# Optimization experiments

Hardware: AMD Instinct MI355X
Metric: run time of the kernel (lower is better)

Reference implementation:

```python
import jax, jax.numpy as jnp
import numpy as np

B, S = 8, 2048
E1, E2, E3 = 256, 256, 512
E = E1 + E2 + E3
NEG_SLOPE = 0.2


def setup_inputs() -> dict:
    key = jax.random.key(0)
    ks = jax.random.split(key, 11)
    scale = 1.0 / np.sqrt(E)
    return {
        "embeding1": jax.random.normal(ks[0], (B, S, E1), jnp.float32),
        "embeding2": jax.random.normal(ks[1], (B, S, E2), jnp.float32),
        "embeding3": jax.random.normal(ks[2], (B, S, E3), jnp.float32),
        # nn.Linear weights are [out, in]; apply as x @ W.T + b
        "Wq": jax.random.uniform(ks[3], (E, E), jnp.float32, -scale, scale),
        "bq": jax.random.uniform(ks[4], (E,), jnp.float32, -scale, scale),
        "Wk": jax.random.uniform(ks[5], (E, E), jnp.float32, -scale, scale),
        "bk": jax.random.uniform(ks[6], (E,), jnp.float32, -scale, scale),
        "Wv": jax.random.uniform(ks[7], (E, E), jnp.float32, -scale, scale),
        "bv": jax.random.uniform(ks[8], (E,), jnp.float32, -scale, scale),
        "Wf": jax.random.uniform(ks[9], (E, E), jnp.float32, -scale, scale),
        "bf": jax.random.uniform(ks[10], (E,), jnp.float32, -scale, scale),
    }


def reference(embeding1, embeding2, embeding3, Wq, bq, Wk, bk, Wv, bv, Wf, bf):
    x = jnp.concatenate([embeding1, embeding2, embeding3], axis=-1)  # [B,S,E]
    q = jnp.einsum("bse,oe->bso", x, Wq) + bq
    k = jnp.einsum("bse,oe->bso", x, Wk) + bk
    v = jnp.einsum("bse,oe->bso", x, Wv) + bv
    # NOTE: no 1/sqrt(d) scaling, faithful to the original module
    scores = jnp.einsum("bqe,bke->bqk", q, k)  # [B,S,S]
    probs = jax.nn.softmax(scores, axis=-1)
    weighted = jnp.einsum("bqk,bke->bqe", probs, v)  # [B,S,E]
    out = jnp.einsum("bse,oe->bso", weighted, Wf) + bf
    return jnp.where(out >= 0, out, NEG_SLOPE * out)
```

## Files before the change

### kernel.cpp

```cpp
#include <hip/hip_runtime.h>
#include <hip/hip_fp16.h>

typedef _Float16 half8 __attribute__((ext_vector_type(8)));
typedef _Float16 half4v __attribute__((ext_vector_type(4)));
typedef float floatx4 __attribute__((ext_vector_type(4)));

__device__ __forceinline__ void load_lds16(const void* g, void* l) {
    __builtin_amdgcn_global_load_lds(
        (const __attribute__((address_space(1))) void*)g,
        (__attribute__((address_space(3))) void*)l,
        16, 0, 0);
}

__device__ __forceinline__ void stage_half(const _Float16* g, long ld, _Float16* dst) {
    const int t = threadIdx.x;
#pragma unroll
    for (int j = 0; j < 2; ++j) {
        const int c = j * 512 + t;
        const int row = c >> 3;
        const int slot = (c & 7) ^ (row & 7);
        load_lds16(g + (long)row * ld + slot * 8, dst + c * 8);
    }
}

#define GEMM_PRELUDE                                                               \
    const int lane = threadIdx.x & 63;                                             \
    const int w    = threadIdx.x >> 6;                                             \
    const int wr   = w >> 2;                                                       \
    const int wc   = w & 3;                                                        \
    const int rsel = lane & 15, gsel = lane >> 4;                                  \
    const int NT = K >> 6;                                                         \
    (void)lane;
#define STAGE(BUF, KT)                                                             \
    stage_half(A + (KT) * 64, lda, lds + (BUF) * 32768);                           \
    stage_half(A + (long)128 * lda + (KT) * 64, lda, lds + (BUF) * 32768 + 8192);  \
    stage_half(B + (KT) * 64, ldb, lds + (BUF) * 32768 + 16384);                   \
    stage_half(B + (long)128 * ldb + (KT) * 64, ldb, lds + (BUF) * 32768 + 24576);
#define READ_A(dst, AH, MH)                                                        \
    _Pragma("unroll") for (int mi = 0; mi < 4; ++mi) {                             \
        const int r = ((MH) * 4 + mi) * 16 + rsel;                                 \
        dst[mi][0] = *(const half8*)&(AH)[r * 64 + ((gsel ^ (r & 7)) << 3)];       \
        dst[mi][1] = *(const half8*)&(AH)[r * 64 + (((4 + gsel) ^ (r & 7)) << 3)]; \
    }
#define READ_B(dst, BH, NH)                                                        \
    _Pragma("unroll") for (int ni = 0; ni < 2; ++ni) {                             \
        const int rn = (wc & 1) * 64 + ((NH) * 2 + ni) * 16 + rsel;                \
        dst[ni][0] = *(const half8*)&(BH)[rn * 64 + ((gsel ^ (rn & 7)) << 3)];     \
        dst[ni][1] = *(const half8*)&(BH)[rn * 64 + (((4 + gsel) ^ (rn & 7)) << 3)]; \
    }
#define MFMA_Q(MH, NH, A_, B_)                                                     \
    _Pragma("unroll") for (int mi = 0; mi < 4; ++mi)                               \
    _Pragma("unroll") for (int ni = 0; ni < 2; ++ni) {                             \
        acc[(MH) * 4 + mi][(NH) * 2 + ni] = __builtin_amdgcn_mfma_f32_16x16x32_f16( \
            A_[mi][0], B_[ni][0], acc[(MH) * 4 + mi][(NH) * 2 + ni], 0, 0, 0);     \
        acc[(MH) * 4 + mi][(NH) * 2 + ni] = __builtin_amdgcn_mfma_f32_16x16x32_f16( \
            A_[mi][1], B_[ni][1], acc[(MH) * 4 + mi][(NH) * 2 + ni], 0, 0, 0);     \
    }
#define SB0 __builtin_amdgcn_sched_barrier(0)

__device__ __forceinline__ void gemm256_core(const _Float16* A, long lda,
                                             const _Float16* B, long ldb,
                                             int K, floatx4 acc[8][4],
                                             _Float16* lds) {
    GEMM_PRELUDE
    half8 a_lo[4][2], a_hi[4][2], b_lo[2][2], b_hi[2][2];
    STAGE(0, 0);
    asm volatile("s_waitcnt vmcnt(0)" ::: "memory");
    __builtin_amdgcn_s_barrier();
    SB0;
#pragma unroll 1
    for (int t = 0; t < NT; ++t) {
        const int buf = t & 1;
        if (t + 1 < NT) { STAGE(buf ^ 1, t + 1); }
        const _Float16* Ah = lds + buf * 32768 + wr * 8192;
        const _Float16* Bh = lds + buf * 32768 + 16384 + (wc >> 1) * 8192;
        READ_A(a_lo, Ah, 0);
        READ_B(b_lo, Bh, 0);
        SB0;
        READ_A(a_hi, Ah, 1);
        SB0;
        READ_B(b_hi, Bh, 1);
        asm volatile("s_waitcnt lgkmcnt(12)" ::: "memory");
        SB0;
        MFMA_Q(0, 0, a_lo, b_lo);
        asm volatile("s_waitcnt lgkmcnt(4)" ::: "memory");
        SB0;
        MFMA_Q(1, 0, a_hi, b_lo);
        asm volatile("s_waitcnt lgkmcnt(0)" ::: "memory");
        SB0;
        MFMA_Q(0, 1, a_lo, b_hi);
        MFMA_Q(1, 1, a_hi, b_hi);
        asm volatile("s_waitcnt vmcnt(0)" ::: "memory");
        __builtin_amdgcn_s_barrier();
        SB0;
    }
}

__device__ __forceinline__ void gemm256_core_pv(const _Float16* A, long lda,
                                                const _Float16* B, long ldb,
                                                int K, floatx4 acc[8][4],
                                                _Float16* lds, const float* scl) {
    GEMM_PRELUDE
    half8 a_lo[4][2], a_hi[4][2], b_lo[2][2], b_hi[2][2];
    STAGE(0, 0);
    asm volatile("s_waitcnt vmcnt(0)" ::: "memory");
    __builtin_amdgcn_s_barrier();
    SB0;
#pragma unroll 1
    for (int t = 0; t < NT; ++t) {
        const int buf = t & 1;
        if (t + 1 < NT) { STAGE(buf ^ 1, t + 1); }
        const _Float16* Ah = lds + buf * 32768 + wr * 8192;
        const _Float16* Bh = lds + buf * 32768 + 16384 + (wc >> 1) * 8192;
        const float* srow = scl + (t >> 2) * 256 + wr * 128 + rsel;
        float s_lo[4], s_hi[4];
#pragma unroll
        for (int mi = 0; mi < 4; ++mi) s_lo[mi] = srow[mi * 16];
#pragma unroll
        for (int mi = 0; mi < 4; ++mi) s_hi[mi] = srow[64 + mi * 16];
        SB0;
        READ_A(a_lo, Ah, 0);
        READ_B(b_lo, Bh, 0);
        SB0;
        READ_A(a_hi, Ah, 1);
        SB0;
        READ_B(b_hi, Bh, 1);
        asm volatile("s_waitcnt lgkmcnt(12)" ::: "memory");
        SB0;
#pragma unroll
        for (int mi = 0; mi < 4; ++mi) {
            const _Float16 h = (_Float16)s_lo[mi];
            a_lo[mi][0] = a_lo[mi][0] * h;
            a_lo[mi][1] = a_lo[mi][1] * h;
        }
        MFMA_Q(0, 0, a_lo, b_lo);
        asm volatile("s_waitcnt lgkmcnt(4)" ::: "memory");
        SB0;
#pragma unroll
        for (int mi = 0; mi < 4; ++mi) {
            const _Float16 h = (_Float16)s_hi[mi];
            a_hi[mi][0] = a_hi[mi][0] * h;
            a_hi[mi][1] = a_hi[mi][1] * h;
        }
        MFMA_Q(1, 0, a_hi, b_lo);
        asm volatile("s_waitcnt lgkmcnt(0)" ::: "memory");
        SB0;
        MFMA_Q(0, 1, a_lo, b_hi);
        MFMA_Q(1, 1, a_hi, b_hi);
        asm volatile("s_waitcnt vmcnt(0)" ::: "memory");
        __builtin_amdgcn_s_barrier();
        SB0;
    }
}

__device__ __forceinline__ void zero_acc8(floatx4 acc[8][4]) {
    const floatx4 z = {0.f, 0.f, 0.f, 0.f};
#pragma unroll
    for (int m = 0; m < 8; ++m)
#pragma unroll
        for (int n = 0; n < 4; ++n) acc[m][n] = z;
}


__global__ __launch_bounds__(256) void prep_kernel(const float* e1, const float* e2,
                                                   const float* e3, const float* Wq,
                                                   const float* Wk, const float* Wv,
                                                   const float* Wf, _Float16* X,
                                                   _Float16* Wdst) {
    const int bid = blockIdx.x;
    if (bid < 16384) {
        long i = ((long)bid * 256 + threadIdx.x) * 4;
        int m = (int)(i >> 10);
        int c = (int)(i & 1023);
        const float* src;
        if (c < 256)      src = e1 + (long)m * 256 + c;
        else if (c < 512) src = e2 + (long)m * 256 + (c - 256);
        else              src = e3 + (long)m * 512 + (c - 512);
        float4 f = *(const float4*)src;
        half4v h;
        h[0] = (_Float16)f.x; h[1] = (_Float16)f.y;
        h[2] = (_Float16)f.z; h[3] = (_Float16)f.w;
        *(half4v*)&X[i] = h;
    } else {
        long i = ((long)(bid - 16384) * 256 + threadIdx.x) * 4;
        int which = (int)(i >> 20);
        long off = i & 1048575;
        const float* w = which == 0 ? Wq : which == 1 ? Wk : which == 2 ? Wv : Wf;
        float4 f = *(const float4*)(w + off);
        half4v h;
        h[0] = (_Float16)f.x; h[1] = (_Float16)f.y;
        h[2] = (_Float16)f.z; h[3] = (_Float16)f.w;
        *(half4v*)&Wdst[i] = h;
    }
}

__global__ __launch_bounds__(512, 2) void qkv_kernel(const _Float16* X, const _Float16* W,
                                                     const float* bq, const float* bk,
                                                     const float* bv, _Float16* q,
                                                     _Float16* k, _Float16* vT) {
    extern __shared__ _Float16 lds[];
    const int m0 = blockIdx.x * 256;
    const int n0 = blockIdx.y * 256;
    const int z  = blockIdx.z;
    floatx4 acc[8][4];
    zero_acc8(acc);
    gemm256_core(X + (long)m0 * 1024, 1024,
                 W + (long)z * 1048576 + (long)n0 * 1024, 1024, 1024, acc, lds);

    const float* bias = (z == 0) ? bq : (z == 1) ? bk : bv;
    const int lane = threadIdx.x & 63;
    const int w = threadIdx.x >> 6;
    const int wr = w >> 2, wc = w & 3;
    const int rsel = lane & 15, gsel = lane >> 4;

    if (z == 2) {
        const int rb = wr * 128 + gsel * 4;
        const int cb = wc * 64 + rsel;
#pragma unroll
        for (int mI = 0; mI < 8; ++mI) {
#pragma unroll
            for (int nI = 0; nI < 4; ++nI) {
                const int c = cb + nI * 16;
                const int r = rb + mI * 16;
                const float bb = bias[n0 + c];
                half4v vv;
#pragma unroll
                for (int j = 0; j < 4; ++j) vv[j] = (_Float16)(acc[mI][nI][j] + bb);
                *(half4v*)&lds[c * 256 + (r ^ ((c & 7) << 3))] = vv;
            }
        }
        __syncthreads();
#pragma unroll
        for (int it = 0; it < 16; ++it) {
            const int idx = it * 512 + threadIdx.x;
            const int c = idx >> 5;
            const int mc = idx & 31;
            half8 v = *(const half8*)&lds[c * 256 + ((mc * 8) ^ ((c & 7) << 3))];
            *(half8*)&vT[(long)(n0 + c) * 16384 + m0 + mc * 8] = v;
        }
    } else {
        _Float16* dst = (z == 0) ? q : k;
        const int r0 = m0 + wr * 128 + gsel * 4;
        const int c0 = n0 + wc * 64 + rsel;
#pragma unroll
        for (int mI = 0; mI < 8; ++mI) {
#pragma unroll
            for (int nI = 0; nI < 4; ++nI) {
                const int r = r0 + mI * 16;
                const int c = c0 + nI * 16;
                const float bb = bias[c];
#pragma unroll
                for (int j = 0; j < 4; ++j)
                    dst[(long)(r + j) * 1024 + c] = (_Float16)(acc[mI][nI][j] + bb);
            }
        }
    }
}

__global__ __launch_bounds__(512, 2) void scores_kernel(const _Float16* qh,
                                                        const _Float16* kh,
                                                        _Float16* es, float* tmax,
                                                        float* tsum) {
    extern __shared__ _Float16 lds[];
    const int m0 = blockIdx.x * 256;
    const int n0 = blockIdx.y * 256;
    const int tile = blockIdx.y;
    const int b = blockIdx.z;
    floatx4 acc[8][4];
    zero_acc8(acc);
    gemm256_core(qh + ((long)b * 2048 + m0) * 1024, 1024,
                 kh + ((long)b * 2048 + n0) * 1024, 1024, 1024, acc, lds);

    const int lane = threadIdx.x & 63;
    const int w = threadIdx.x >> 6;
    const int wr = w >> 2, wc = w & 3;
    const int rsel = lane & 15, gsel = lane >> 4;
    float* red = (float*)lds;

    float mx[8][4];
#pragma unroll
    for (int m = 0; m < 8; ++m)
#pragma unroll
        for (int j = 0; j < 4; ++j) {
            float v = acc[m][0][j];
#pragma unroll
            for (int n = 1; n < 4; ++n) v = fmaxf(v, acc[m][n][j]);
#pragma unroll
            for (int d = 1; d < 16; d <<= 1) v = fmaxf(v, __shfl_xor(v, d));
            mx[m][j] = v;
        }
    if (rsel == 0) {
#pragma unroll
        for (int m = 0; m < 8; ++m)
#pragma unroll
            for (int j = 0; j < 4; ++j)
                red[(wr * 128 + m * 16 + gsel * 4 + j) * 4 + wc] = mx[m][j];
    }
    __syncthreads();
#pragma unroll
    for (int m = 0; m < 8; ++m)
#pragma unroll
        for (int j = 0; j < 4; ++j) {
            const int row = wr * 128 + m * 16 + gsel * 4 + j;
            float4 rv = *(const float4*)&red[row * 4];
            mx[m][j] = fmaxf(fmaxf(rv.x, rv.y), fmaxf(rv.z, rv.w));
        }
    __syncthreads();

    float sm[8][4];
#pragma unroll
    for (int m = 0; m < 8; ++m)
#pragma unroll
        for (int j = 0; j < 4; ++j) {
            float s = 0.f;
#pragma unroll
            for (int n = 0; n < 4; ++n) {
                float e = __expf(acc[m][n][j] - mx[m][j]);
                acc[m][n][j] = e;
                s += e;
            }
#pragma unroll
            for (int d = 1; d < 16; d <<= 1) s += __shfl_xor(s, d);
            sm[m][j] = s;
        }
    if (rsel == 0) {
#pragma unroll
        for (int m = 0; m < 8; ++m)
#pragma unroll
            for (int j = 0; j < 4; ++j)
                red[(wr * 128 + m * 16 + gsel * 4 + j) * 4 + wc] = sm[m][j];
    }
    __syncthreads();
    if (wc == 0 && rsel == 0) {
        const long base = ((long)b * 8 + tile) * 2048 + m0;
#pragma unroll
        for (int m = 0; m < 8; ++m)
#pragma unroll
            for (int j = 0; j < 4; ++j) {
                const int row = wr * 128 + m * 16 + gsel * 4 + j;
                float4 rv = *(const float4*)&red[row * 4];
                tmax[base + row] = mx[m][j];
                tsum[base + row] = rv.x + rv.y + rv.z + rv.w;
            }
    }
    const long rbase = (long)b * 2048 * 2048;
    const int r0 = m0 + wr * 128 + gsel * 4;
    const int c0 = n0 + wc * 64 + rsel;
#pragma unroll
    for (int m = 0; m < 8; ++m)
#pragma unroll
        for (int n = 0; n < 4; ++n)
#pragma unroll
            for (int j = 0; j < 4; ++j)
                es[rbase + (long)(r0 + m * 16 + j) * 2048 + c0 + n * 16] =
                    (_Float16)acc[m][n][j];
}

__global__ __launch_bounds__(256) void sm_reduce_kernel(const float* tmax,
                                                        const float* tsum,
                                                        float* scale) {
    const int idx = blockIdx.x * 256 + threadIdx.x;
    const int b = idx >> 11, row = idx & 2047;
    const float* mrow = tmax + (long)b * 8 * 2048 + row;
    const float* srow = tsum + (long)b * 8 * 2048 + row;
    float m[8];
    float mg = -1e30f;
#pragma unroll
    for (int t = 0; t < 8; ++t) {
        m[t] = mrow[(long)t * 2048];
        mg = fmaxf(mg, m[t]);
    }
    float Z = 0.f;
#pragma unroll
    for (int t = 0; t < 8; ++t) Z += srow[(long)t * 2048] * __expf(m[t] - mg);
    const float inv = 1.0f / Z;
    float* orow = scale + (long)b * 8 * 2048 + row;
#pragma unroll
    for (int t = 0; t < 8; ++t) orow[(long)t * 2048] = __expf(m[t] - mg) * inv;
}

__global__ __launch_bounds__(512, 2) void pv_kernel(const _Float16* es,
                                                    const _Float16* vT,
                                                    const float* scale_g,
                                                    _Float16* wt) {
    extern __shared__ _Float16 lds[];
    const int m0 = blockIdx.x * 256;
    const int n0 = blockIdx.y * 256;
    const int batch = blockIdx.z;
    float* scl = (float*)(lds + 65536);
    for (int i = threadIdx.x; i < 2048; i += 512) {
        const int t8 = i >> 8, rl = i & 255;
        scl[i] = scale_g[((long)batch * 8 + t8) * 2048 + m0 + rl];
    }
    __syncthreads();
    floatx4 acc[8][4];
    zero_acc8(acc);
    gemm256_core_pv(es + ((long)batch * 2048 + m0) * 2048, 2048,
                    vT + (long)n0 * 16384 + (long)batch * 2048, 16384, 2048, acc,
                    lds, scl);

    const int lane = threadIdx.x & 63;
    const int w = threadIdx.x >> 6;
    const int wr = w >> 2, wc = w & 3;
    const int r0 = wr * 128 + (lane >> 4) * 4;
    const int c0 = n0 + wc * 64 + (lane & 15);
#pragma unroll
    for (int m = 0; m < 8; ++m) {
#pragma unroll
        for (int n = 0; n < 4; ++n) {
            const int r = r0 + m * 16;
            const int c = c0 + n * 16;
#pragma unroll
            for (int j = 0; j < 4; ++j)
                wt[((long)batch * 2048 + m0 + r + j) * 1024 + c] =
                    (_Float16)acc[m][n][j];
        }
    }
}

__global__ __launch_bounds__(512, 2) void out_kernel(const _Float16* wt, const _Float16* Wf,
                                                     const float* bf_, float* out) {
    extern __shared__ _Float16 lds[];
    const int m0 = blockIdx.x * 256;
    const int n0 = blockIdx.y * 256;
    floatx4 acc[8][4];
    zero_acc8(acc);
    gemm256_core(wt + (long)m0 * 1024, 1024, Wf + (long)n0 * 1024, 1024, 1024, acc, lds);

    const int lane = threadIdx.x & 63;
    const int w = threadIdx.x >> 6;
    const int wr = w >> 2, wc = w & 3;
    const int r0 = m0 + wr * 128 + (lane >> 4) * 4;
    const int c0 = n0 + wc * 64 + (lane & 15);
#pragma unroll
    for (int m = 0; m < 8; ++m) {
#pragma unroll
        for (int n = 0; n < 4; ++n) {
            const int r = r0 + m * 16;
            const int c = c0 + n * 16;
            const float bb = bf_[c];
#pragma unroll
            for (int j = 0; j < 4; ++j) {
                float y = acc[m][n][j] + bb;
                y = (y >= 0.f) ? y : 0.2f * y;
                out[(long)(r + j) * 1024 + c] = y;
            }
        }
    }
}

extern "C" void kernel_launch(void* const* d_in, const int* in_sizes, int n_in,
                              void* d_out, int out_size, void* d_ws, size_t ws_size,
                              hipStream_t stream) {
    const float* e1 = (const float*)d_in[0];
    const float* e2 = (const float*)d_in[1];
    const float* e3 = (const float*)d_in[2];
    const float* Wq = (const float*)d_in[3];
    const float* bq = (const float*)d_in[4];
    const float* Wk = (const float*)d_in[5];
    const float* bk = (const float*)d_in[6];
    const float* Wv = (const float*)d_in[7];
    const float* bv = (const float*)d_in[8];
    const float* Wf = (const float*)d_in[9];
    const float* bf_ = (const float*)d_in[10];
    float* out = (float*)d_out;

    const int LDS_BYTES = 131072;
    const int LDS_PV = 131072 + 8192;
    (void)hipFuncSetAttribute((const void*)qkv_kernel,
                              hipFuncAttributeMaxDynamicSharedMemorySize, LDS_BYTES);
    (void)hipFuncSetAttribute((const void*)scores_kernel,
                              hipFuncAttributeMaxDynamicSharedMemorySize, LDS_BYTES);
    (void)hipFuncSetAttribute((const void*)pv_kernel,
                              hipFuncAttributeMaxDynamicSharedMemorySize, LDS_PV);
    (void)hipFuncSetAttribute((const void*)out_kernel,
                              hipFuncAttributeMaxDynamicSharedMemorySize, LDS_BYTES);

    char* ws = (char*)d_ws;
    const size_t MB = 1024 * 1024;
    _Float16* Xh    = (_Float16*)(ws + 0);
    _Float16* Wh    = (_Float16*)(ws + 32 * MB);
    _Float16* qh    = (_Float16*)(ws + 40 * MB);
    _Float16* kh    = (_Float16*)(ws + 72 * MB);
    _Float16* vT    = (_Float16*)(ws + 104 * MB);
    _Float16* wt    = (_Float16*)(ws + 136 * MB);
    _Float16* es    = (_Float16*)(ws + 168 * MB);
    float* tmax     = (float*)(ws + 232 * MB);
    float* tsum     = (float*)(ws + 232 * MB + 524288);
    float* scale    = (float*)(ws + 233 * MB);

    prep_kernel<<<20480, 256, 0, stream>>>(e1, e2, e3, Wq, Wk, Wv, Wf, Xh, Wh);
    qkv_kernel<<<dim3(64, 4, 3), 512, LDS_BYTES, stream>>>(Xh, Wh, bq, bk, bv, qh, kh, vT);
    scores_kernel<<<dim3(8, 8, 8), 512, LDS_BYTES, stream>>>(qh, kh, es, tmax, tsum);
    sm_reduce_kernel<<<64, 256, 0, stream>>>(tmax, tsum, scale);
    pv_kernel<<<dim3(8, 4, 8), 512, LDS_PV, stream>>>(es, vT, scale, wt);
    out_kernel<<<dim3(64, 4), 512, LDS_BYTES, stream>>>(wt, Wh + 3 * 1048576, bf_, out);
}
```

Measured before the change: 367.9 us.

## Stage score tile through LDS for coalesced stores and remap grid batch-fastest

The scores kernel now transposes its fp16 accumulator tile through swizzled LDS so each thread writes 16-byte contiguous chunks of the score matrix, replacing scattered 2-byte stores. Both the scores and PV kernels also remap the block index so the batch dimension varies fastest across blocks, which changes which blocks run concurrently and may help L2/MALL locality across XCDs. This adds an extra LDS round trip and a barrier in the scores epilogue.

```diff
diff --git a/kernel.cpp b/kernel.cpp
--- a/kernel.cpp
+++ b/kernel.cpp
@@ -262,10 +262,10 @@
                                                         _Float16* es, float* tmax,
                                                         float* tsum) {
     extern __shared__ _Float16 lds[];
-    const int m0 = blockIdx.x * 256;
-    const int n0 = blockIdx.y * 256;
-    const int tile = blockIdx.y;
-    const int b = blockIdx.z;
+    const int b = blockIdx.x;
+    const int m0 = (blockIdx.y >> 3) * 256;
+    const int tile = blockIdx.y & 7;
+    const int n0 = tile * 256;
     floatx4 acc[8][4];
     zero_acc8(acc);
     gemm256_core(qh + ((long)b * 2048 + m0) * 1024, 1024,
@@ -343,17 +343,37 @@
                 tsum[base + row] = rv.x + rv.y + rv.z + rv.w;
             }
     }
+    __syncthreads();
+
+#pragma unroll
+    for (int m = 0; m < 8; ++m) {
+        const int r = wr * 128 + m * 16 + gsel * 4;
+#pragma unroll
+        for (int n = 0; n < 4; ++n) {
+            const int c = wc * 64 + n * 16 + rsel;
+            const int s = (c & 7) ^ ((c >> 3) & 7);
+            half4v hv;
+#pragma unroll
+            for (int j = 0; j < 4; ++j) hv[j] = (_Float16)acc[m][n][j];
+            *(half4v*)&lds[c * 256 + (r ^ (s << 3))] = hv;
+        }
+    }
+    __syncthreads();
     const long rbase = (long)b * 2048 * 2048;
-    const int r0 = m0 + wr * 128 + gsel * 4;
-    const int c0 = n0 + wc * 64 + rsel;
-#pragma unroll
-    for (int m = 0; m < 8; ++m)
-#pragma unroll
-        for (int n = 0; n < 4; ++n)
-#pragma unroll
-            for (int j = 0; j < 4; ++j)
-                es[rbase + (long)(r0 + m * 16 + j) * 2048 + c0 + n * 16] =
-                    (_Float16)acc[m][n][j];
+#pragma unroll
+    for (int it = 0; it < 16; ++it) {
+        const int idx = it * 512 + threadIdx.x;
+        const int r = idx >> 5;
+        const int chunk = idx & 31;
+        half8 h;
+#pragma unroll
+        for (int e = 0; e < 8; ++e) {
+            const int c = chunk * 8 + e;
+            const int s = e ^ (chunk & 7);
+            h[e] = lds[c * 256 + (r ^ (s << 3))];
+        }
+        *(half8*)&es[rbase + (long)(m0 + r) * 2048 + n0 + chunk * 8] = h;
+    }
 }
 
 __global__ __launch_bounds__(256) void sm_reduce_kernel(const float* tmax,
@@ -384,9 +404,9 @@
                                                     const float* scale_g,
                                                     _Float16* wt) {
     extern __shared__ _Float16 lds[];
-    const int m0 = blockIdx.x * 256;
-    const int n0 = blockIdx.y * 256;
-    const int batch = blockIdx.z;
+    const int batch = blockIdx.x;
+    const int m0 = (blockIdx.y >> 2) * 256;
+    const int n0 = (blockIdx.y & 3) * 256;
     float* scl = (float*)(lds + 65536);
     for (int i = threadIdx.x; i < 2048; i += 512) {
         const int t8 = i >> 8, rl = i & 255;
@@ -491,8 +511,8 @@
 
     prep_kernel<<<20480, 256, 0, stream>>>(e1, e2, e3, Wq, Wk, Wv, Wf, Xh, Wh);
     qkv_kernel<<<dim3(64, 4, 3), 512, LDS_BYTES, stream>>>(Xh, Wh, bq, bk, bv, qh, kh, vT);
-    scores_kernel<<<dim3(8, 8, 8), 512, LDS_BYTES, stream>>>(qh, kh, es, tmax, tsum);
+    scores_kernel<<<dim3(8, 64), 512, LDS_BYTES, stream>>>(qh, kh, es, tmax, tsum);
     sm_reduce_kernel<<<64, 256, 0, stream>>>(tmax, tsum, scale);
-    pv_kernel<<<dim3(8, 4, 8), 512, LDS_PV, stream>>>(es, vT, scale, wt);
+    pv_kernel<<<dim3(8, 32), 512, LDS_PV, stream>>>(es, vT, scale, wt);
     out_kernel<<<dim3(64, 4), 512, LDS_BYTES, stream>>>(wt, Wh + 3 * 1048576, bf_, out);
 }
```

After: 363.7 us. Within noise of the previous version (-1.1%).
